# Performance work log

Hardware: AMD Instinct MI355X
Metric: run time of the kernel (lower is better)

## Reference

```python
import jax, jax.numpy as jnp
import numpy as np

EPS = 1e-6


def setup_inputs() -> dict:
    key = jax.random.key(0)
    k1, k2, k3, k4 = jax.random.split(key, 4)
    B, L, H, E = 16, 4096, 8, 64
    return {
        "queries": jax.random.normal(k1, (B, L, H, E), dtype=jnp.float32),
        "keys": jax.random.normal(k2, (B, L, H, E), dtype=jnp.float32),
        "values": jax.random.normal(k3, (B, L, H, E), dtype=jnp.float32),
        "attn_mask": jnp.ones((1,), dtype=bool),
        "gamma": jax.random.uniform(k4, (1,), dtype=jnp.float32),
    }


def reference(queries, keys, values, attn_mask, gamma):
    # Faithful to the original: keys/values/attn_mask are unused; Q=K=V=queries.
    B, L, H, E = queries.shape
    HE = H * E
    V = queries.reshape(B, L, HE)              # raw values [B, L, HE]
    # l2_norm: normalize over dim=-2 (the L axis)
    Qn = V / jnp.linalg.norm(V, axis=-2, keepdims=True)   # [B, L, HE]
    Kt = jnp.swapaxes(Qn, -1, -2)              # K = l2_norm(K).permute -> [B, HE, L]
    # tailor_sum: 1 / (HE + sum_n Kt[b,n,l] * (sum_l' Qn[b,l',n] + eps))  -> [B, L]
    q_colsum = jnp.sum(Qn, axis=-2) + EPS      # [B, HE]
    tailor = 1.0 / (HE + jnp.einsum('bnl,bn->bl', Kt, q_colsum))  # [B, L]
    # value_sum over L, broadcast to [B, L, HE]
    value_sum = jnp.sum(V, axis=-2)            # [B, HE]
    # (V @ K) @ Q == V @ (K @ Q): use the linear-complexity [HE,HE] inner matrix
    KQ = jnp.einsum('bnl,blm->bnm', Kt, Qn)    # [B, HE, HE]
    part = jnp.einsum('bln,bnm->blm', V, KQ)   # [B, L, HE]
    matrix_sum = value_sum[:, None, :] + part  # [B, L, HE]
    weight_value = (matrix_sum * tailor[:, :, None]).reshape(B, L, H, E)
    return queries + gamma * weight_value
```

## Files before the change

### kernel.cpp

```cpp
#include <hip/hip_runtime.h>

#define EPS 1e-6f
#define LL 4096
#define HE 512

typedef __attribute__((ext_vector_type(8))) short short8;
typedef __attribute__((ext_vector_type(4))) float f32x4;

__device__ __forceinline__ unsigned short f2bf(float f) {
    union { float f; unsigned u; } v; v.f = f;
    unsigned r = v.u + 0x7FFFu + ((v.u >> 16) & 1u);
    return (unsigned short)(r >> 16);
}
__device__ __forceinline__ float bf2f(unsigned short s) {
    union { unsigned u; float f; } v; v.u = ((unsigned)s) << 16;
    return v.f;
}
__device__ __forceinline__ void gl16(const unsigned short* g, unsigned short* l) {
    __builtin_amdgcn_global_load_lds(
        (const __attribute__((address_space(1))) unsigned int*)(const void*)g,
        (__attribute__((address_space(3))) unsigned int*)(void*)l,
        16, 0, 0);
}

__global__ __launch_bounds__(256) void k1_fuse2(const float* __restrict__ q,
        unsigned short* __restrict__ Vb, unsigned short* __restrict__ Vt,
        float* __restrict__ ps, float* __restrict__ pq) {
    __shared__ unsigned short ldsT[256][68];
    __shared__ float lds_s[4][512];
    __shared__ float lds_q[4][512];
    int blk = blockIdx.x;
    int b = blk >> 6, lt = blk & 63;
    int t = threadIdx.x;
    int oct = t & 63, w = t >> 6;
    size_t rowbase = (size_t)b * LL + lt * 64 + w * 16;
    const float* qb = q + rowbase * HE + oct * 8;
    unsigned short* vb = Vb + rowbase * HE + oct * 8;
    short8 rows[16];
    float s[8] = {}, qq[8] = {};
    #pragma unroll
    for (int r = 0; r < 16; r++) {
        float4 v0 = *(const float4*)(qb + (size_t)r * HE);
        float4 v1 = *(const float4*)(qb + (size_t)r * HE + 4);
        unsigned short e[8] = {f2bf(v0.x), f2bf(v0.y), f2bf(v0.z), f2bf(v0.w),
                               f2bf(v1.x), f2bf(v1.y), f2bf(v1.z), f2bf(v1.w)};
        short8 w8;
        #pragma unroll
        for (int c = 0; c < 8; c++) {
            w8[c] = (short)e[c];
            float x = bf2f(e[c]);
            s[c] += x; qq[c] += x * x;
        }
        rows[r] = w8;
        *(short8*)(vb + (size_t)r * HE) = w8;
    }
    #pragma unroll
    for (int c = 0; c < 8; c++) {
        lds_s[w][oct * 8 + c] = s[c];
        lds_q[w][oct * 8 + c] = qq[c];
    }
    __syncthreads();
    #pragma unroll
    for (int h = 0; h < 2; h++) {
        int col = h * 256 + t;
        float ss = lds_s[0][col] + lds_s[1][col] + lds_s[2][col] + lds_s[3][col];
        float sq = lds_q[0][col] + lds_q[1][col] + lds_q[2][col] + lds_q[3][col];
        ps[(size_t)lt * 8192 + b * 512 + col] = ss;
        pq[(size_t)lt * 8192 + b * 512 + col] = sq;
    }
    int gg = (t & 63) >> 3, oo = t & 7;
    #pragma unroll
    for (int h = 0; h < 2; h++) {
        __syncthreads();
        if ((oct >> 5) == h) {
            int ol = oct & 31;
            #pragma unroll
            for (int c = 0; c < 8; c++) {
                int n1 = ol * 8 + c;
                int swz = (ol & 7) * 8;
                #pragma unroll
                for (int g = 0; g < 4; g++) {
                    uint2 dv;
                    dv.x = (unsigned)(unsigned short)rows[g*4+0][c]
                         | ((unsigned)(unsigned short)rows[g*4+1][c] << 16);
                    dv.y = (unsigned)(unsigned short)rows[g*4+2][c]
                         | ((unsigned)(unsigned short)rows[g*4+3][c] << 16);
                    int lp = (w * 16 + g * 4) ^ swz;
                    *(uint2*)&ldsT[n1][lp] = dv;
                }
            }
        }
        __syncthreads();
        #pragma unroll
        for (int it = 0; it < 8; it++) {
            int n1 = w * 64 + it * 8 + gg;
            int swz = ((n1 >> 3) & 7) * 8;
            int l0 = oo * 8;
            uint2 a0 = *(const uint2*)&ldsT[n1][(l0    ) ^ swz];
            uint2 a1 = *(const uint2*)&ldsT[n1][(l0 + 4) ^ swz];
            uint4 uv; uv.x = a0.x; uv.y = a0.y; uv.z = a1.x; uv.w = a1.y;
            unsigned short* dst = Vt + ((size_t)b * HE + h * 256 + n1) * LL + lt * 64 + l0;
            *(uint4*)dst = uv;
        }
    }
}

__global__ __launch_bounds__(256) void k2_reduce(const float* __restrict__ ps,
        const float* __restrict__ pq, float* __restrict__ sumV,
        float* __restrict__ cvec, float* __restrict__ invn) {
    int i = blockIdx.x * 256 + threadIdx.x;
    float s = 0.f, qq = 0.f;
    #pragma unroll 8
    for (int lt = 0; lt < 64; lt++) {
        s  += ps[(size_t)lt * 8192 + i];
        qq += pq[(size_t)lt * 8192 + i];
    }
    float inv = 1.0f / sqrtf(qq);
    sumV[i] = s;
    invn[i] = inv;
    cvec[i] = (s * inv + EPS) * inv;
}

__global__ __launch_bounds__(256) void k3_dvec(const unsigned short* __restrict__ Vb,
        const float* __restrict__ cvec, float* __restrict__ dvec) {
    int blk = blockIdx.x;
    int b = blk >> 7, lblk = blk & 127;
    int t = threadIdx.x;
    int lloc = t >> 3, j = t & 7;
    int l = lblk * 32 + lloc;
    const unsigned short* rowp = Vb + ((size_t)b * LL + l) * HE + j * 64;
    const float* cp = cvec + b * HE + j * 64;
    float d = 0.f;
    #pragma unroll
    for (int g = 0; g < 8; g++) {
        short8 v = *(const short8*)(rowp + g * 8);
        float4 c0 = *(const float4*)(cp + g * 8);
        float4 c1 = *(const float4*)(cp + g * 8 + 4);
        d += bf2f((unsigned short)v[0]) * c0.x + bf2f((unsigned short)v[1]) * c0.y
           + bf2f((unsigned short)v[2]) * c0.z + bf2f((unsigned short)v[3]) * c0.w
           + bf2f((unsigned short)v[4]) * c1.x + bf2f((unsigned short)v[5]) * c1.y
           + bf2f((unsigned short)v[6]) * c1.z + bf2f((unsigned short)v[7]) * c1.w;
    }
    d += __shfl_xor(d, 1); d += __shfl_xor(d, 2); d += __shfl_xor(d, 4);
    if (j == 0) dvec[(size_t)b * LL + l] = d;
}

__global__ __launch_bounds__(256) void k4_gram(const unsigned short* __restrict__ Vt,
        unsigned short* __restrict__ Gp) {
    __shared__ __attribute__((aligned(16))) unsigned short la[2][128][64];
    __shared__ __attribute__((aligned(16))) unsigned short lb[2][128][64];
    int cpx = gridDim.x >> 3;
    int blk = ((int)blockIdx.x & 7) * cpx + ((int)blockIdx.x >> 3);
    int b = blk / 80;
    int rem = blk - b * 80;
    int pair = rem >> 3, split = rem & 7;
    int nt = (pair < 4) ? 0 : (pair < 7) ? 1 : (pair < 9) ? 2 : 3;
    int off = (nt * (9 - nt)) >> 1;
    int mt = nt + pair - off;
    bool diag = (nt == mt);
    int N0 = nt * 128, M0 = mt * 128;
    int t = threadIdx.x;
    int w = t >> 6, lane = t & 63;
    int wr = w >> 1, wc = w & 1;
    int rl = lane >> 3;
    int cl = ((lane & 7) ^ rl) << 3;
    int lr = lane & 15, q4 = lane >> 4;
    int ch0 = (q4 ^ (lane & 7)) << 3;
    const unsigned short* pa = Vt + ((size_t)b * HE + N0) * LL + split * 512;
    const unsigned short* pb = Vt + ((size_t)b * HE + M0) * LL + split * 512;
    f32x4 acc[4][4] = {};

#define STAGE4(B, KB) do { \
    int _k0 = (KB) * 64; \
    _Pragma("unroll") \
    for (int p = 0; p < 4; p++) { \
        int r0 = p * 32 + w * 8; \
        gl16(pa + (size_t)(r0 + rl) * LL + _k0 + cl, &la[B][r0][0]); \
        if (!diag) gl16(pb + (size_t)(r0 + rl) * LL + _k0 + cl, &lb[B][r0][0]); \
    } } while (0)

    STAGE4(0, 0);
    #pragma unroll
    for (int kb = 0; kb < 8; kb++) {
        int cur = kb & 1;
        if (kb < 7) {
            STAGE4(cur ^ 1, kb + 1);
            if (diag) { asm volatile("s_waitcnt vmcnt(4)" ::: "memory"); }
            else      { asm volatile("s_waitcnt vmcnt(8)" ::: "memory"); }
        } else {
            asm volatile("s_waitcnt vmcnt(0)" ::: "memory");
        }
        __builtin_amdgcn_s_barrier();
        const unsigned short (*A)[64] = la[cur];
        const unsigned short (*Bp)[64] = diag ? la[cur] : lb[cur];
        #pragma unroll
        for (int ks = 0; ks < 2; ks++) {
            int colA = ch0 ^ (ks << 5);
            short8 af[4], bfr[4];
            #pragma unroll
            for (int i = 0; i < 4; i++)
                af[i] = *(const short8*)&A[wr*64 + i*16 + lr][colA];
            #pragma unroll
            for (int j = 0; j < 4; j++)
                bfr[j] = *(const short8*)&Bp[wc*64 + j*16 + lr][colA];
            #pragma unroll
            for (int i = 0; i < 4; i++)
                #pragma unroll
                for (int j = 0; j < 4; j++)
                    acc[i][j] = __builtin_amdgcn_mfma_f32_16x16x32_bf16(af[i], bfr[j], acc[i][j], 0, 0, 0);
        }
        __builtin_amdgcn_s_barrier();
    }
#undef STAGE4
    size_t tbase = ((size_t)(b * 10 + pair) * 8 + split) * 16384;
    #pragma unroll
    for (int i = 0; i < 4; i++) {
        int nb = wr*64 + i*16 + q4*4;
        #pragma unroll
        for (int j = 0; j < 4; j++) {
            int ml = wc*64 + j*16 + lr;
            ushort4 wv;
            wv.x = f2bf(acc[i][j][0]); wv.y = f2bf(acc[i][j][1]);
            wv.z = f2bf(acc[i][j][2]); wv.w = f2bf(acc[i][j][3]);
            *(ushort4*)&Gp[tbase + (size_t)ml * 128 + nb] = wv;
        }
    }
}

__global__ __launch_bounds__(256) void k5_reduce(const unsigned short* __restrict__ Gp,
        const float* __restrict__ invn, unsigned short* __restrict__ KQb) {
    __shared__ unsigned short lds_t[128][130];
    int blk = blockIdx.x;
    int b = blk / 10, pair = blk % 10;
    int nt = (pair < 4) ? 0 : (pair < 7) ? 1 : (pair < 9) ? 2 : 3;
    int off = (nt * (9 - nt)) >> 1;
    int mt = nt + pair - off;
    int N0 = nt * 128, M0 = mt * 128;
    int t = threadIdx.x;
    const unsigned short* gp = Gp + ((size_t)(b * 10 + pair) * 8) * 16384;
    const float* inb = invn + (size_t)b * HE;
    #pragma unroll 2
    for (int e = 0; e < 32; e++) {
        int idx = e * 512 + t * 2;
        int ml = idx >> 7, nl = idx & 127;
        float s0 = 0.f, s1 = 0.f;
        #pragma unroll
        for (int sp = 0; sp < 8; sp++) {
            unsigned g2 = *(const unsigned*)&gp[(size_t)sp * 16384 + idx];
            s0 += bf2f((unsigned short)(g2 & 0xFFFF));
            s1 += bf2f((unsigned short)(g2 >> 16));
        }
        float im = inb[M0 + ml];
        ushort2 v;
        v.x = f2bf(s0 * inb[N0 + nl] * im);
        v.y = f2bf(s1 * inb[N0 + nl + 1] * im);
        *(ushort2*)&KQb[((size_t)b * HE + M0 + ml) * HE + N0 + nl] = v;
        *(ushort2*)&lds_t[ml][nl] = v;
    }
    __syncthreads();
    #pragma unroll 2
    for (int e = 0; e < 32; e++) {
        int idx = e * 512 + t * 2;
        int nl = idx >> 7, ml = idx & 127;
        ushort2 v;
        v.x = lds_t[ml][nl];
        v.y = lds_t[ml + 1][nl];
        *(ushort2*)&KQb[((size_t)b * HE + N0 + nl) * HE + M0 + ml] = v;
    }
}

__global__ __launch_bounds__(256) void k6_part(const unsigned short* __restrict__ KQb,
        const unsigned short* __restrict__ Vb, const float* __restrict__ dvec,
        const float* __restrict__ sumV, const float* __restrict__ gamma,
        float* __restrict__ out) {
    __shared__ __attribute__((aligned(16))) unsigned short la[2][128][64];
    __shared__ __attribute__((aligned(16))) unsigned short lb[2][128][64];
    int cpx = gridDim.x >> 3;
    int blk = ((int)blockIdx.x & 7) * cpx + ((int)blockIdx.x >> 3);
    int b = blk >> 7, mt = (blk >> 5) & 3, lt = blk & 31;
    int M0 = mt * 128, L0 = lt * 128;
    int t = threadIdx.x;
    int w = t >> 6, lane = t & 63;
    int wr = w >> 1, wc = w & 1;
    int rl = lane >> 3;
    int cl = ((lane & 7) ^ rl) << 3;
    int lr = lane & 15, q4 = lane >> 4;
    int ch0 = (q4 ^ (lane & 7)) << 3;
    const unsigned short* pa = KQb + ((size_t)b * HE + M0) * HE;
    const unsigned short* pb = Vb + ((size_t)b * LL + L0) * HE;
    float gma = gamma[0];
    f32x4 acc[4][4] = {};

#define STAGE6(B, KB) do { \
    int _k0 = (KB) * 64; \
    _Pragma("unroll") \
    for (int p = 0; p < 4; p++) { \
        int r0 = p * 32 + w * 8; \
        gl16(pa + (size_t)(r0 + rl) * HE + _k0 + cl, &la[B][r0][0]); \
        gl16(pb + (size_t)(r0 + rl) * HE + _k0 + cl, &lb[B][r0][0]); \
    } } while (0)

    STAGE6(0, 0);
    #pragma unroll
    for (int kb = 0; kb < 8; kb++) {
        int cur = kb & 1;
        if (kb < 7) {
            STAGE6(cur ^ 1, kb + 1);
            asm volatile("s_waitcnt vmcnt(8)" ::: "memory");
        } else {
            asm volatile("s_waitcnt vmcnt(0)" ::: "memory");
        }
        __builtin_amdgcn_s_barrier();
        #pragma unroll
        for (int ks = 0; ks < 2; ks++) {
            int colA = ch0 ^ (ks << 5);
            short8 af[4], bfr[4];
            #pragma unroll
            for (int i = 0; i < 4; i++)
                af[i] = *(const short8*)&la[cur][wr*64 + i*16 + lr][colA];
            #pragma unroll
            for (int j = 0; j < 4; j++)
                bfr[j] = *(const short8*)&lb[cur][wc*64 + j*16 + lr][colA];
            #pragma unroll
            for (int i = 0; i < 4; i++)
                #pragma unroll
                for (int j = 0; j < 4; j++)
                    acc[i][j] = __builtin_amdgcn_mfma_f32_16x16x32_bf16(af[i], bfr[j], acc[i][j], 0, 0, 0);
        }
        __builtin_amdgcn_s_barrier();
    }
#undef STAGE6
    #pragma unroll
    for (int j = 0; j < 4; j++) {
        int lglob = L0 + wc*64 + j*16 + lr;
        float dt = dvec[(size_t)b * LL + lglob];
        float tailor = 1.0f / (512.0f + dt);
        #pragma unroll
        for (int i = 0; i < 4; i++) {
            int m4 = M0 + wr*64 + i*16 + q4*4;
            size_t ofs = ((size_t)b * LL + lglob) * HE + m4;
            ushort4 rv = *(const ushort4*)(Vb + ((size_t)b * LL + lglob) * HE + m4);
            float4 vs = *(const float4*)(sumV + (size_t)b * HE + m4);
            float4 o;
            o.x = bf2f(rv.x) + gma * (vs.x + acc[i][j][0]) * tailor;
            o.y = bf2f(rv.y) + gma * (vs.y + acc[i][j][1]) * tailor;
            o.z = bf2f(rv.z) + gma * (vs.z + acc[i][j][2]) * tailor;
            o.w = bf2f(rv.w) + gma * (vs.w + acc[i][j][3]) * tailor;
            *(float4*)(out + ofs) = o;
        }
    }
}

extern "C" void kernel_launch(void* const* d_in, const int* in_sizes, int n_in,
                              void* d_out, int out_size, void* d_ws, size_t ws_size,
                              hipStream_t stream) {
    const float* q     = (const float*)d_in[0];
    const float* gamma = (const float*)d_in[4];
    float* out = (float*)d_out;
    char* ws = (char*)d_ws;
    float* sumV  = (float*)(ws);
    float* cvec  = (float*)(ws + 65536);
    float* invn  = (float*)(ws + 98304);
    float* dvec  = (float*)(ws + 131072);
    unsigned short* KQb = (unsigned short*)(ws + 524288);
    unsigned short* Vt  = (unsigned short*)(ws + 8912896);
    unsigned short* Vb  = (unsigned short*)(ws + 76021760);
    unsigned short* Gp  = (unsigned short*)(ws + 143130624);
    float* ps = (float*)(ws + 185073664);
    float* pq = (float*)(ws + 187170816);

    k1_fuse2 <<<1024, 256, 0, stream>>>(q, Vb, Vt, ps, pq);
    k2_reduce<<<32,   256, 0, stream>>>(ps, pq, sumV, cvec, invn);
    k3_dvec  <<<2048, 256, 0, stream>>>(Vb, cvec, dvec);
    k4_gram  <<<1280, 256, 0, stream>>>(Vt, Gp);
    k5_reduce<<<160,  256, 0, stream>>>(Gp, invn, KQb);
    k6_part  <<<2048, 256, 0, stream>>>(KQb, Vb, dvec, sumV, gamma, out);
}
```

Measured before the change: 209.5 us.

## Halve k1 row slab to 32 rows, shrink shared memory, stage partials in output

The first kernel now handles 32-row slabs instead of 64, so it launches twice as many blocks. Each thread keeps 8 bf16 rows in registers instead of 16, and the transpose buffer shares one aliased shared-memory region with the reduction arrays. The intent is higher occupancy and more parallel work for the cast and transpose pass. The cost is twice as many partial-sum rows for k2 to reduce and shorter 64-byte contiguous writes into Vt. Partial sums now live in the output buffer as scratch, which depends on k6 overwriting it afterwards.

```diff
diff --git a/kernel.cpp b/kernel.cpp
--- a/kernel.cpp
+++ b/kernel.cpp
@@ -23,23 +23,24 @@
         16, 0, 0);
 }
 
-__global__ __launch_bounds__(256) void k1_fuse2(const float* __restrict__ q,
+__global__ __launch_bounds__(256) void k1_fuse3(const float* __restrict__ q,
         unsigned short* __restrict__ Vb, unsigned short* __restrict__ Vt,
         float* __restrict__ ps, float* __restrict__ pq) {
-    __shared__ unsigned short ldsT[256][68];
-    __shared__ float lds_s[4][512];
-    __shared__ float lds_q[4][512];
+    __shared__ __attribute__((aligned(16))) char smem[512 * 36 * 2];
+    float (*lds_s)[512] = (float (*)[512])smem;
+    float (*lds_q)[512] = (float (*)[512])(smem + 8192);
+    unsigned short (*ldsT)[36] = (unsigned short (*)[36])smem;
     int blk = blockIdx.x;
-    int b = blk >> 6, lt = blk & 63;
-    int t = threadIdx.x;
-    int oct = t & 63, w = t >> 6;
-    size_t rowbase = (size_t)b * LL + lt * 64 + w * 16;
-    const float* qb = q + rowbase * HE + oct * 8;
-    unsigned short* vb = Vb + rowbase * HE + oct * 8;
-    short8 rows[16];
+    int b = blk >> 7, slab = blk & 127;
+    int t = threadIdx.x;
+    int w = t >> 6, oct = t & 63;
+    int row0 = slab * 32 + w * 8;
+    const float* qb = q + ((size_t)b * LL + row0) * HE + oct * 8;
+    unsigned short* vb = Vb + ((size_t)b * LL + row0) * HE + oct * 8;
+    short8 rows8[8];
     float s[8] = {}, qq[8] = {};
     #pragma unroll
-    for (int r = 0; r < 16; r++) {
+    for (int r = 0; r < 8; r++) {
         float4 v0 = *(const float4*)(qb + (size_t)r * HE);
         float4 v1 = *(const float4*)(qb + (size_t)r * HE + 4);
         unsigned short e[8] = {f2bf(v0.x), f2bf(v0.y), f2bf(v0.z), f2bf(v0.w),
@@ -51,7 +52,7 @@
             float x = bf2f(e[c]);
             s[c] += x; qq[c] += x * x;
         }
-        rows[r] = w8;
+        rows8[r] = w8;
         *(short8*)(vb + (size_t)r * HE) = w8;
     }
     #pragma unroll
@@ -65,42 +66,41 @@
         int col = h * 256 + t;
         float ss = lds_s[0][col] + lds_s[1][col] + lds_s[2][col] + lds_s[3][col];
         float sq = lds_q[0][col] + lds_q[1][col] + lds_q[2][col] + lds_q[3][col];
-        ps[(size_t)lt * 8192 + b * 512 + col] = ss;
-        pq[(size_t)lt * 8192 + b * 512 + col] = sq;
-    }
-    int gg = (t & 63) >> 3, oo = t & 7;
-    #pragma unroll
-    for (int h = 0; h < 2; h++) {
-        __syncthreads();
-        if ((oct >> 5) == h) {
-            int ol = oct & 31;
-            #pragma unroll
-            for (int c = 0; c < 8; c++) {
-                int n1 = ol * 8 + c;
-                int swz = (ol & 7) * 8;
-                #pragma unroll
-                for (int g = 0; g < 4; g++) {
-                    uint2 dv;
-                    dv.x = (unsigned)(unsigned short)rows[g*4+0][c]
-                         | ((unsigned)(unsigned short)rows[g*4+1][c] << 16);
-                    dv.y = (unsigned)(unsigned short)rows[g*4+2][c]
-                         | ((unsigned)(unsigned short)rows[g*4+3][c] << 16);
-                    int lp = (w * 16 + g * 4) ^ swz;
-                    *(uint2*)&ldsT[n1][lp] = dv;
-                }
-            }
-        }
-        __syncthreads();
-        #pragma unroll
-        for (int it = 0; it < 8; it++) {
-            int n1 = w * 64 + it * 8 + gg;
-            int swz = ((n1 >> 3) & 7) * 8;
-            int l0 = oo * 8;
-            uint2 a0 = *(const uint2*)&ldsT[n1][(l0    ) ^ swz];
-            uint2 a1 = *(const uint2*)&ldsT[n1][(l0 + 4) ^ swz];
-            uint4 uv; uv.x = a0.x; uv.y = a0.y; uv.z = a1.x; uv.w = a1.y;
-            unsigned short* dst = Vt + ((size_t)b * HE + h * 256 + n1) * LL + lt * 64 + l0;
-            *(uint4*)dst = uv;
+        ps[(size_t)slab * 8192 + b * 512 + col] = ss;
+        pq[(size_t)slab * 8192 + b * 512 + col] = sq;
+    }
+    __syncthreads();
+    int swz = (oct & 7) * 4;
+    #pragma unroll
+    for (int c = 0; c < 8; c++) {
+        int n1 = oct * 8 + c;
+        #pragma unroll
+        for (int g = 0; g < 2; g++) {
+            int lp = (w * 8 + g * 4) ^ swz;
+            uint2 dv;
+            dv.x = (unsigned)(unsigned short)rows8[g*4+0][c]
+                 | ((unsigned)(unsigned short)rows8[g*4+1][c] << 16);
+            dv.y = (unsigned)(unsigned short)rows8[g*4+2][c]
+                 | ((unsigned)(unsigned short)rows8[g*4+3][c] << 16);
+            *(uint2*)&ldsT[n1][lp] = dv;
+        }
+    }
+    __syncthreads();
+    #pragma unroll
+    for (int i = 0; i < 2; i++) {
+        int n = t + i * 256;
+        int nswz = ((n >> 3) & 7) * 4;
+        uint2 ck[8];
+        #pragma unroll
+        for (int k = 0; k < 8; k++)
+            ck[k] = *(const uint2*)&ldsT[n][(k * 4) ^ nswz];
+        unsigned short* dst = Vt + ((size_t)b * HE + n) * LL + slab * 32;
+        #pragma unroll
+        for (int k = 0; k < 4; k++) {
+            uint4 uv;
+            uv.x = ck[2*k].x; uv.y = ck[2*k].y;
+            uv.z = ck[2*k+1].x; uv.w = ck[2*k+1].y;
+            *(uint4*)(dst + k * 8) = uv;
         }
     }
 }
@@ -111,7 +111,7 @@
     int i = blockIdx.x * 256 + threadIdx.x;
     float s = 0.f, qq = 0.f;
     #pragma unroll 8
-    for (int lt = 0; lt < 64; lt++) {
+    for (int lt = 0; lt < 128; lt++) {
         s  += ps[(size_t)lt * 8192 + i];
         qq += pq[(size_t)lt * 8192 + i];
     }
@@ -366,10 +366,10 @@
     unsigned short* Vt  = (unsigned short*)(ws + 8912896);
     unsigned short* Vb  = (unsigned short*)(ws + 76021760);
     unsigned short* Gp  = (unsigned short*)(ws + 143130624);
-    float* ps = (float*)(ws + 185073664);
-    float* pq = (float*)(ws + 187170816);
-
-    k1_fuse2 <<<1024, 256, 0, stream>>>(q, Vb, Vt, ps, pq);
+    float* ps = (float*)d_out;
+    float* pq = (float*)d_out + 1048576;
+
+    k1_fuse3 <<<2048, 256, 0, stream>>>(q, Vb, Vt, ps, pq);
     k2_reduce<<<32,   256, 0, stream>>>(ps, pq, sumV, cvec, invn);
     k3_dvec  <<<2048, 256, 0, stream>>>(Vb, cvec, dvec);
     k4_gram  <<<1280, 256, 0, stream>>>(Vt, Gp);
```

Measured after the change: 234.3 us. +11.8%, slower.
